# Kernel optimization log

Hardware: AMD Instinct MI355X
Metric: run time of the kernel (lower is better)

The kernel has to match this reference:

```python
import jax, jax.numpy as jnp
import numpy as np

D = 1024
H = 16
DEPTH = D // H


def setup_inputs() -> dict:
    key = jax.random.key(0)
    ks = jax.random.split(key, 9)
    s = 1.0 / np.sqrt(D)
    return {
        "x": jax.random.normal(ks[0], (2, 2048, D), dtype=jnp.float32),
        "Wq": jax.random.uniform(ks[1], (D, D), jnp.float32, -s, s),
        "bq": jax.random.uniform(ks[2], (D,), jnp.float32, -s, s),
        "Wk": jax.random.uniform(ks[3], (D, D), jnp.float32, -s, s),
        "bk": jax.random.uniform(ks[4], (D,), jnp.float32, -s, s),
        "Wv": jax.random.uniform(ks[5], (D, D), jnp.float32, -s, s),
        "bv": jax.random.uniform(ks[6], (D,), jnp.float32, -s, s),
        "Wo": jax.random.uniform(ks[7], (D, D), jnp.float32, -s, s),
        "bo": jax.random.uniform(ks[8], (D,), jnp.float32, -s, s),
    }


def _split_heads(t):
    b, s, _ = t.shape
    return t.reshape(b, s, H, DEPTH).transpose(0, 2, 1, 3)  # [B,H,S,depth]


def reference(x, Wq, bq, Wk, bk, Wv, bv, Wo, bo):
    q = _split_heads(x @ Wq.T + bq)
    k = _split_heads(x @ Wk.T + bk)
    v = _split_heads(x @ Wv.T + bv)
    scores = jnp.einsum("bhqd,bhkd->bhqk", q, k) / jnp.sqrt(jnp.float32(DEPTH))
    weights = jax.nn.softmax(scores, axis=-1)
    attn = jnp.einsum("bhqk,bhkd->bhqd", weights, v)
    b, _, s, _ = attn.shape
    attn = attn.transpose(0, 2, 1, 3).reshape(b, s, D)
    return attn @ Wo.T + bo
```

## Files before the change

### kernel.cpp

```cpp
#include <hip/hip_runtime.h>
#include <hip/hip_bf16.h>


typedef __bf16 bf16x8 __attribute__((ext_vector_type(8)));
typedef float f32x4 __attribute__((ext_vector_type(4)));
typedef unsigned short u16;
typedef unsigned short u16x4 __attribute__((ext_vector_type(4)));
typedef unsigned short u16x8 __attribute__((ext_vector_type(8)));
typedef unsigned int u32x2 __attribute__((ext_vector_type(2)));

__device__ __forceinline__ u16 f2bf(float f) {
  union { float f; unsigned u; } x; x.f = f;
  return (u16)((x.u + 0x7fffu + ((x.u >> 16) & 1u)) >> 16);
}

__device__ __forceinline__ void load_lds16(const void* g, void* l) {
  __builtin_amdgcn_global_load_lds((const __attribute__((address_space(1))) void*)g,
                                   (__attribute__((address_space(3))) void*)l,
                                   16, 0, 0);
}

__device__ __forceinline__ bf16x8 frag128(const u16* base, int row, int ch) {
  return *(const bf16x8*)((const char*)base + row * 128 + (((ch) ^ (row & 7)) << 4));
}

__device__ __forceinline__ float exp2_hw(float x) {
  float r;
  asm("v_exp_f32 %0, %1" : "=v"(r) : "v"(x));
  return r;
}

__device__ __forceinline__ unsigned cvt_pk_bf16(float lo, float hi) {
  unsigned r;
  asm("v_cvt_pk_bf16_f32 %0, %1, %2" : "=v"(r) : "v"(lo), "v"(hi));
  return r;
}

__device__ __forceinline__ bf16x8 mk8(unsigned a, unsigned b, unsigned c,
                                      unsigned d) {
  union { unsigned u[4]; bf16x8 v; } x;
  x.u[0] = a; x.u[1] = b; x.u[2] = c; x.u[3] = d;
  return x.v;
}

__global__ __launch_bounds__(256) void cvt_all(
    const float* __restrict__ x, const float* __restrict__ wq,
    const float* __restrict__ wk, const float* __restrict__ wv,
    const float* __restrict__ wo, u16* __restrict__ dst) {
  int i = blockIdx.x * 256 + threadIdx.x;
  const float* src;
  int loc;
  if (i < 1048576) {
    src = x; loc = i;
  } else {
    int j = i - 1048576;
    int seg = j >> 18;
    loc = j & 262143;
    src = (seg == 0) ? wq : (seg == 1) ? wk : (seg == 2) ? wv : wo;
  }
  f32x4 v = ((const f32x4*)src)[loc];
  u16x4 o;
#pragma unroll
  for (int j = 0; j < 4; ++j) o[j] = f2bf(v[j]);
  ((u16x4*)dst)[i] = o;
}

template <int BM, int MODE>
__global__ __launch_bounds__(256) void gemm_bf16(
    const u16* __restrict__ A, const u16* __restrict__ Bw,
    const float* __restrict__ bias0, const float* __restrict__ bias1,
    const float* __restrict__ bias2,
    u16* __restrict__ o_q, u16* __restrict__ o_k, u16* __restrict__ o_vt,
    float* __restrict__ o_f, int K) {
  constexpr int MBF = BM / 32;
  constexpr int NBX = (MODE == 0) ? 24 : 8;
  constexpr int NBY = (MODE == 0) ? 32 : 64;
  __shared__ u16 sA[BM * 64];
  __shared__ u16 sB[128 * 64];
  const int tid = threadIdx.x, l = tid & 63, w = tid >> 6;
  const int wr = w >> 1, wc = w & 1;
  const int lr = l & 15, lq = l >> 4;
  const int lin = blockIdx.y * NBX + blockIdx.x;
  const int wgs = (lin & 7) * (NBX * NBY / 8) + (lin >> 3);
  const int m0 = (wgs / NBX) * BM, n0 = (wgs % NBX) * 128;

  f32x4 acc[MBF][4];
#pragma unroll
  for (int mb = 0; mb < MBF; ++mb)
#pragma unroll
    for (int nb = 0; nb < 4; ++nb) acc[mb][nb] = f32x4{0.f, 0.f, 0.f, 0.f};

  const int nkt = K / 64;
  for (int kt = 0; kt < nkt; ++kt) {
#pragma unroll
    for (int i = 0; i < BM / 32; ++i) {
      int p = (i * 4 + w) * 1024 + l * 16;
      int row = p >> 7, ch = ((p >> 4) & 7) ^ (row & 7);
      load_lds16(A + (size_t)(m0 + row) * K + kt * 64 + ch * 8,
                 (char*)sA + (i * 4 + w) * 1024);
    }
#pragma unroll
    for (int i = 0; i < 4; ++i) {
      int p = (i * 4 + w) * 1024 + l * 16;
      int row = p >> 7, ch = ((p >> 4) & 7) ^ (row & 7);
      load_lds16(Bw + (size_t)(n0 + row) * K + kt * 64 + ch * 8,
                 (char*)sB + (i * 4 + w) * 1024);
    }
    __syncthreads();
#pragma unroll
    for (int ks = 0; ks < 2; ++ks) {
      bf16x8 af[MBF], bfr[4];
#pragma unroll
      for (int mb = 0; mb < MBF; ++mb)
        af[mb] = frag128(sA, wr * (BM / 2) + mb * 16 + lr, lq + 4 * ks);
#pragma unroll
      for (int nb = 0; nb < 4; ++nb)
        bfr[nb] = frag128(sB, wc * 64 + nb * 16 + lr, lq + 4 * ks);
#pragma unroll
      for (int mb = 0; mb < MBF; ++mb)
#pragma unroll
        for (int nb = 0; nb < 4; ++nb)
          acc[mb][nb] = __builtin_amdgcn_mfma_f32_16x16x32_bf16(
              af[mb], bfr[nb], acc[mb][nb], 0, 0, 0);
    }
    __syncthreads();
  }

#pragma unroll
  for (int nb = 0; nb < 4; ++nb) {
    const int n = n0 + wc * 64 + nb * 16 + lr;
    if constexpr (MODE == 0) {
      const int qkv = n >> 10, c = n & 1023;
      const float* bp = (qkv == 0) ? bias0 : ((qkv == 1) ? bias1 : bias2);
      const float bv = bp[c];
      const int h = c >> 6, d = c & 63;
      if (qkv == 2) {
#pragma unroll
        for (int mb = 0; mb < MBF; ++mb) {
          int mbase = m0 + wr * (BM / 2) + mb * 16 + lq * 4;
          int b = mbase >> 11, s0 = mbase & 2047;
          int pos0 = (s0 & ~31) | (((s0 >> 2) & 3) << 3) | (((s0 >> 4) & 1) << 2);
          u16x4 pk;
#pragma unroll
          for (int r = 0; r < 4; ++r) pk[r] = f2bf(acc[mb][nb][r] + bv);
          *(u16x4*)(o_vt + ((size_t)((b * 16 + h) * 64 + d)) * 2048 + pos0) = pk;
        }
      } else {
        u16* dp = (qkv == 0) ? o_q : o_k;
#pragma unroll
        for (int mb = 0; mb < MBF; ++mb)
#pragma unroll
          for (int r = 0; r < 4; ++r) {
            int m = m0 + wr * (BM / 2) + mb * 16 + lq * 4 + r;
            int b = m >> 11, s = m & 2047;
            float v = acc[mb][nb][r] + bv;
            if (qkv == 0) v *= 0.18033688011f;
            dp[((size_t)(b * 16 + h) * 2048 + s) * 64 + d] = f2bf(v);
          }
      }
    } else {
      const float bv = bias0[n];
#pragma unroll
      for (int mb = 0; mb < MBF; ++mb)
#pragma unroll
        for (int r = 0; r < 4; ++r) {
          int m = m0 + wr * (BM / 2) + mb * 16 + lq * 4 + r;
          o_f[(size_t)m * 1024 + n] = acc[mb][nb][r] + bv;
        }
    }
  }
}

__global__ __launch_bounds__(256, 2) void attn_fwd(
    const u16* __restrict__ q16, const u16* __restrict__ k16,
    const u16* __restrict__ vt16, u16* __restrict__ att16) {
  __shared__ u16 sK[2][128 * 64];
  __shared__ u16 sV[2][64 * 128];
  const int tid = threadIdx.x, l = tid & 63, w = tid >> 6;
  const int lr = l & 15, lq = l >> 4;
  const int lin = (blockIdx.y << 4) | blockIdx.x;
  const int wg = (lin & 7) * 64 + (lin >> 3);
  const int qt = wg & 15, bh = wg >> 4;
  const int b = bh >> 4, h = bh & 15;
  const char* kg = (const char*)(k16 + (size_t)bh * 2048 * 64);
  const char* vg = (const char*)(vt16 + (size_t)bh * 64 * 2048);

  bf16x8 aq[2][2];
#pragma unroll
  for (int mb = 0; mb < 2; ++mb)
#pragma unroll
    for (int ks = 0; ks < 2; ++ks) {
      int qrow = qt * 128 + w * 32 + mb * 16 + lr;
      aq[mb][ks] = *(const bf16x8*)(q16 + ((size_t)bh * 2048 + qrow) * 64 +
                                    ks * 32 + lq * 8);
    }

  int koff[4], voff[4];
#pragma unroll
  for (int i = 0; i < 4; ++i) {
    int p = (i * 4 + w) * 1024 + l * 16;
    int krow = p >> 7, kch = ((p >> 4) & 7) ^ (krow & 7);
    koff[i] = krow * 128 + kch * 16;
    int vrow = p >> 8, vch = ((p >> 4) & 15) ^ (vrow & 7);
    voff[i] = vrow * 4096 + vch * 16;
  }

#pragma unroll
  for (int i = 0; i < 4; ++i)
    load_lds16(kg + koff[i], (char*)sK[0] + (i * 4 + w) * 1024);
#pragma unroll
  for (int i = 0; i < 4; ++i)
    load_lds16(vg + voff[i], (char*)sV[0] + (i * 4 + w) * 1024);
  __syncthreads();

  f32x4 o[2][4];
#pragma unroll
  for (int mb = 0; mb < 2; ++mb)
#pragma unroll
    for (int db = 0; db < 4; ++db) o[mb][db] = f32x4{0.f, 0.f, 0.f, 0.f};
  float l_run[2] = {0.f, 0.f};

  for (int kt = 0; kt < 16; ++kt) {
    const int cur = kt & 1;
    const u16* sKc = sK[cur];
    const u16* sVc = sV[cur];

    if (kt < 15) {
      char* dK = (char*)sK[cur ^ 1];
      char* dV = (char*)sV[cur ^ 1];
#pragma unroll
      for (int i = 0; i < 4; ++i)
        load_lds16(kg + (size_t)(kt + 1) * 16384 + koff[i],
                   dK + (i * 4 + w) * 1024);
#pragma unroll
      for (int i = 0; i < 4; ++i)
        load_lds16(vg + (size_t)(kt + 1) * 256 + voff[i],
                   dV + (i * 4 + w) * 1024);
    }

    f32x4 s[2][8];
#pragma unroll
    for (int mb = 0; mb < 2; ++mb)
#pragma unroll
      for (int nb = 0; nb < 8; ++nb) s[mb][nb] = f32x4{0.f, 0.f, 0.f, 0.f};
    __builtin_amdgcn_s_setprio(1);
#pragma unroll
    for (int ks = 0; ks < 2; ++ks) {
#pragma unroll
      for (int g = 0; g < 2; ++g) {
        bf16x8 bk[4];
#pragma unroll
        for (int j = 0; j < 4; ++j)
          bk[j] = frag128(sKc, (g * 4 + j) * 16 + lr, lq + 4 * ks);
#pragma unroll
        for (int j = 0; j < 4; ++j)
#pragma unroll
          for (int mb = 0; mb < 2; ++mb)
            s[mb][g * 4 + j] = __builtin_amdgcn_mfma_f32_16x16x32_bf16(
                bk[j], aq[mb][ks], s[mb][g * 4 + j], 0, 0, 0);
      }
    }
    __builtin_amdgcn_s_setprio(0);

#pragma unroll
    for (int mb = 0; mb < 2; ++mb) {
      float rs = 0.f;
#pragma unroll
      for (int nb = 0; nb < 8; ++nb)
#pragma unroll
        for (int r = 0; r < 4; ++r) {
          float p_ = exp2_hw(s[mb][nb][r]);
          s[mb][nb][r] = p_;
          rs += p_;
        }
      l_run[mb] += rs;
    }

#pragma unroll
    for (int g = 0; g < 4; ++g) {
      bf16x8 ap[2];
#pragma unroll
      for (int mb = 0; mb < 2; ++mb)
        ap[mb] = mk8(cvt_pk_bf16(s[mb][2 * g][0], s[mb][2 * g][1]),
                     cvt_pk_bf16(s[mb][2 * g][2], s[mb][2 * g][3]),
                     cvt_pk_bf16(s[mb][2 * g + 1][0], s[mb][2 * g + 1][1]),
                     cvt_pk_bf16(s[mb][2 * g + 1][2], s[mb][2 * g + 1][3]));
      bf16x8 bv[4];
#pragma unroll
      for (int db = 0; db < 4; ++db) {
        int row = db * 16 + lr;
        bv[db] = *(const bf16x8*)((const char*)sVc + row * 256 +
                                  (((4 * g + lq) ^ (row & 7)) << 4));
      }
      __builtin_amdgcn_s_setprio(1);
#pragma unroll
      for (int db = 0; db < 4; ++db)
#pragma unroll
        for (int mb = 0; mb < 2; ++mb)
          o[mb][db] = __builtin_amdgcn_mfma_f32_16x16x32_bf16(
              ap[mb], bv[db], o[mb][db], 0, 0, 0);
      __builtin_amdgcn_s_setprio(0);
    }

    __syncthreads();
  }

#pragma unroll
  for (int mb = 0; mb < 2; ++mb) {
    float lv = l_run[mb];
    lv += __shfl_xor(lv, 16, 64);
    lv += __shfl_xor(lv, 32, 64);
    float inv[4];
#pragma unroll
    for (int r = 0; r < 4; ++r) inv[r] = 1.f / __shfl(lv, lq * 4 + r, 64);
#pragma unroll
    for (int db = 0; db < 4; ++db)
#pragma unroll
      for (int r = 0; r < 4; ++r) {
        float v = o[mb][db][r] * inv[r];
        int qg_ = qt * 128 + w * 32 + mb * 16 + lq * 4 + r;
        int col = h * 64 + db * 16 + lr;
        att16[((size_t)(b * 2048 + qg_)) * 1024 + col] = f2bf(v);
      }
  }
}

extern "C" void kernel_launch(void* const* d_in, const int* in_sizes, int n_in,
                              void* d_out, int out_size, void* d_ws, size_t ws_size,
                              hipStream_t stream) {
  const float* x  = (const float*)d_in[0];
  const float* Wq = (const float*)d_in[1];
  const float* bq = (const float*)d_in[2];
  const float* Wk = (const float*)d_in[3];
  const float* bk = (const float*)d_in[4];
  const float* Wv = (const float*)d_in[5];
  const float* bv = (const float*)d_in[6];
  const float* Wo = (const float*)d_in[7];
  const float* bo = (const float*)d_in[8];
  float* out = (float*)d_out;

  char* ws = (char*)d_ws;
  const size_t MB = 1024 * 1024;
  if (ws_size < 40 * MB) return;
  u16* x16  = (u16*)(ws);
  u16* w16  = (u16*)(ws + 8 * MB);
  u16* q16  = (u16*)(ws + 16 * MB);
  u16* k16  = (u16*)(ws + 24 * MB);
  u16* vt16 = (u16*)(ws + 32 * MB);
  u16* att16 = x16;

  cvt_all<<<8192, 256, 0, stream>>>(x, Wq, Wk, Wv, Wo, x16);

  gemm_bf16<128, 0><<<dim3(24, 32), 256, 0, stream>>>(
      x16, w16, bq, bk, bv, q16, k16, vt16, nullptr, 1024);

  attn_fwd<<<dim3(16, 32), 256, 0, stream>>>(q16, k16, vt16, att16);

  gemm_bf16<64, 1><<<dim3(8, 64), 256, 0, stream>>>(
      att16, w16 + 3145728, bo, nullptr, nullptr, nullptr, nullptr, nullptr,
      out, 1024);
}
```

Measured before the change: 107.5 us.

## Software-pipeline attention loop: overlap PV of previous tile with QK of current

```diff
diff --git a/kernel.cpp b/kernel.cpp
--- a/kernel.cpp
+++ b/kernel.cpp
@@ -175,7 +175,7 @@
     const u16* __restrict__ q16, const u16* __restrict__ k16,
     const u16* __restrict__ vt16, u16* __restrict__ att16) {
   __shared__ u16 sK[2][128 * 64];
-  __shared__ u16 sV[2][64 * 128];
+  __shared__ u16 sV[3][64 * 128];
   const int tid = threadIdx.x, l = tid & 63, w = tid >> 6;
   const int lr = l & 15, lq = l >> 4;
   const int lin = (blockIdx.y << 4) | blockIdx.x;
@@ -219,24 +219,23 @@
 #pragma unroll
     for (int db = 0; db < 4; ++db) o[mb][db] = f32x4{0.f, 0.f, 0.f, 0.f};
   float l_run[2] = {0.f, 0.f};
-
-  for (int kt = 0; kt < 16; ++kt) {
-    const int cur = kt & 1;
-    const u16* sKc = sK[cur];
-    const u16* sVc = sV[cur];
-
-    if (kt < 15) {
-      char* dK = (char*)sK[cur ^ 1];
-      char* dV = (char*)sV[cur ^ 1];
+  bf16x8 pE[2][4], pO[2][4];
+
+#pragma unroll
+  for (int t = 0; t < 16; ++t) {
+    if (t < 15) {
+      char* dK = (char*)sK[(t + 1) & 1];
+      char* dV = (char*)sV[(t + 1) % 3];
 #pragma unroll
       for (int i = 0; i < 4; ++i)
-        load_lds16(kg + (size_t)(kt + 1) * 16384 + koff[i],
+        load_lds16(kg + (size_t)(t + 1) * 16384 + koff[i],
                    dK + (i * 4 + w) * 1024);
 #pragma unroll
       for (int i = 0; i < 4; ++i)
-        load_lds16(vg + (size_t)(kt + 1) * 256 + voff[i],
+        load_lds16(vg + (size_t)(t + 1) * 256 + voff[i],
                    dV + (i * 4 + w) * 1024);
     }
+    const u16* sKc = sK[t & 1];
 
     f32x4 s[2][8];
 #pragma unroll
@@ -261,6 +260,29 @@
       }
     }
     __builtin_amdgcn_s_setprio(0);
+
+    if (t > 0) {
+      const u16* sVp = sV[(t - 1) % 3];
+#pragma unroll
+      for (int g = 0; g < 4; ++g) {
+        bf16x8 bv[4];
+#pragma unroll
+        for (int db = 0; db < 4; ++db) {
+          int row = db * 16 + lr;
+          bv[db] = *(const bf16x8*)((const char*)sVp + row * 256 +
+                                    (((4 * g + lq) ^ (row & 7)) << 4));
+        }
+        __builtin_amdgcn_s_setprio(1);
+#pragma unroll
+        for (int db = 0; db < 4; ++db)
+#pragma unroll
+          for (int mb = 0; mb < 2; ++mb)
+            o[mb][db] = __builtin_amdgcn_mfma_f32_16x16x32_bf16(
+                ((t - 1) & 1) ? pO[mb][g] : pE[mb][g], bv[db], o[mb][db],
+                0, 0, 0);
+        __builtin_amdgcn_s_setprio(0);
+      }
+    }
 
 #pragma unroll
     for (int mb = 0; mb < 2; ++mb) {
@@ -274,35 +296,37 @@
           rs += p_;
         }
       l_run[mb] += rs;
-    }
-
+#pragma unroll
+      for (int g = 0; g < 4; ++g) {
+        bf16x8 pk = mk8(cvt_pk_bf16(s[mb][2 * g][0], s[mb][2 * g][1]),
+                        cvt_pk_bf16(s[mb][2 * g][2], s[mb][2 * g][3]),
+                        cvt_pk_bf16(s[mb][2 * g + 1][0], s[mb][2 * g + 1][1]),
+                        cvt_pk_bf16(s[mb][2 * g + 1][2], s[mb][2 * g + 1][3]));
+        if (t & 1) pO[mb][g] = pk; else pE[mb][g] = pk;
+      }
+    }
+
+    __syncthreads();
+  }
+
+  {
+    const u16* sVp = sV[0];
 #pragma unroll
     for (int g = 0; g < 4; ++g) {
-      bf16x8 ap[2];
-#pragma unroll
-      for (int mb = 0; mb < 2; ++mb)
-        ap[mb] = mk8(cvt_pk_bf16(s[mb][2 * g][0], s[mb][2 * g][1]),
-                     cvt_pk_bf16(s[mb][2 * g][2], s[mb][2 * g][3]),
-                     cvt_pk_bf16(s[mb][2 * g + 1][0], s[mb][2 * g + 1][1]),
-                     cvt_pk_bf16(s[mb][2 * g + 1][2], s[mb][2 * g + 1][3]));
       bf16x8 bv[4];
 #pragma unroll
       for (int db = 0; db < 4; ++db) {
         int row = db * 16 + lr;
-        bv[db] = *(const bf16x8*)((const char*)sVc + row * 256 +
+        bv[db] = *(const bf16x8*)((const char*)sVp + row * 256 +
                                   (((4 * g + lq) ^ (row & 7)) << 4));
       }
-      __builtin_amdgcn_s_setprio(1);
 #pragma unroll
       for (int db = 0; db < 4; ++db)
 #pragma unroll
         for (int mb = 0; mb < 2; ++mb)
           o[mb][db] = __builtin_amdgcn_mfma_f32_16x16x32_bf16(
-              ap[mb], bv[db], o[mb][db], 0, 0, 0);
-      __builtin_amdgcn_s_setprio(0);
-    }
-
-    __syncthreads();
+              pO[mb][g], bv[db], o[mb][db], 0, 0, 0);
+    }
   }
 
 #pragma unroll
```

New measurement: 415.4 us. 3.87x slower.

## Split key tile into halves and interleave QK^T of second half with PV of first

Applied to the files above, without the earlier changes.

```diff
diff --git a/kernel.cpp b/kernel.cpp
--- a/kernel.cpp
+++ b/kernel.cpp
@@ -238,69 +238,121 @@
                    dV + (i * 4 + w) * 1024);
     }
 
-    f32x4 s[2][8];
+    f32x4 sA[2][4];
 #pragma unroll
     for (int mb = 0; mb < 2; ++mb)
 #pragma unroll
-      for (int nb = 0; nb < 8; ++nb) s[mb][nb] = f32x4{0.f, 0.f, 0.f, 0.f};
+      for (int nb = 0; nb < 4; ++nb) sA[mb][nb] = f32x4{0.f, 0.f, 0.f, 0.f};
     __builtin_amdgcn_s_setprio(1);
 #pragma unroll
     for (int ks = 0; ks < 2; ++ks) {
-#pragma unroll
-      for (int g = 0; g < 2; ++g) {
-        bf16x8 bk[4];
-#pragma unroll
-        for (int j = 0; j < 4; ++j)
-          bk[j] = frag128(sKc, (g * 4 + j) * 16 + lr, lq + 4 * ks);
-#pragma unroll
-        for (int j = 0; j < 4; ++j)
-#pragma unroll
-          for (int mb = 0; mb < 2; ++mb)
-            s[mb][g * 4 + j] = __builtin_amdgcn_mfma_f32_16x16x32_bf16(
-                bk[j], aq[mb][ks], s[mb][g * 4 + j], 0, 0, 0);
-      }
+      bf16x8 bk[4];
+#pragma unroll
+      for (int j = 0; j < 4; ++j)
+        bk[j] = frag128(sKc, j * 16 + lr, lq + 4 * ks);
+#pragma unroll
+      for (int j = 0; j < 4; ++j)
+#pragma unroll
+        for (int mb = 0; mb < 2; ++mb)
+          sA[mb][j] = __builtin_amdgcn_mfma_f32_16x16x32_bf16(
+              bk[j], aq[mb][ks], sA[mb][j], 0, 0, 0);
     }
     __builtin_amdgcn_s_setprio(0);
 
+    bf16x8 pA[2][2];
 #pragma unroll
     for (int mb = 0; mb < 2; ++mb) {
       float rs = 0.f;
 #pragma unroll
-      for (int nb = 0; nb < 8; ++nb)
+      for (int nb = 0; nb < 4; ++nb)
 #pragma unroll
         for (int r = 0; r < 4; ++r) {
-          float p_ = exp2_hw(s[mb][nb][r]);
-          s[mb][nb][r] = p_;
+          float p_ = exp2_hw(sA[mb][nb][r]);
+          sA[mb][nb][r] = p_;
           rs += p_;
         }
       l_run[mb] += rs;
-    }
-
-#pragma unroll
-    for (int g = 0; g < 4; ++g) {
-      bf16x8 ap[2];
-#pragma unroll
-      for (int mb = 0; mb < 2; ++mb)
-        ap[mb] = mk8(cvt_pk_bf16(s[mb][2 * g][0], s[mb][2 * g][1]),
-                     cvt_pk_bf16(s[mb][2 * g][2], s[mb][2 * g][3]),
-                     cvt_pk_bf16(s[mb][2 * g + 1][0], s[mb][2 * g + 1][1]),
-                     cvt_pk_bf16(s[mb][2 * g + 1][2], s[mb][2 * g + 1][3]));
+#pragma unroll
+      for (int g = 0; g < 2; ++g)
+        pA[mb][g] = mk8(cvt_pk_bf16(sA[mb][2 * g][0], sA[mb][2 * g][1]),
+                        cvt_pk_bf16(sA[mb][2 * g][2], sA[mb][2 * g][3]),
+                        cvt_pk_bf16(sA[mb][2 * g + 1][0], sA[mb][2 * g + 1][1]),
+                        cvt_pk_bf16(sA[mb][2 * g + 1][2], sA[mb][2 * g + 1][3]));
+    }
+
+    f32x4 sB[2][4];
+#pragma unroll
+    for (int mb = 0; mb < 2; ++mb)
+#pragma unroll
+      for (int nb = 0; nb < 4; ++nb) sB[mb][nb] = f32x4{0.f, 0.f, 0.f, 0.f};
+    __builtin_amdgcn_s_setprio(1);
+#pragma unroll
+    for (int ks = 0; ks < 2; ++ks) {
+      bf16x8 bk[4];
+#pragma unroll
+      for (int j = 0; j < 4; ++j)
+        bk[j] = frag128(sKc, (4 + j) * 16 + lr, lq + 4 * ks);
+      bf16x8 bvA[4];
+#pragma unroll
+      for (int db = 0; db < 4; ++db) {
+        int row = db * 16 + lr;
+        bvA[db] = *(const bf16x8*)((const char*)sVc + row * 256 +
+                                   (((4 * ks + lq) ^ (row & 7)) << 4));
+      }
+#pragma unroll
+      for (int j = 0; j < 4; ++j)
+#pragma unroll
+        for (int mb = 0; mb < 2; ++mb)
+          sB[mb][j] = __builtin_amdgcn_mfma_f32_16x16x32_bf16(
+              bk[j], aq[mb][ks], sB[mb][j], 0, 0, 0);
+#pragma unroll
+      for (int db = 0; db < 4; ++db)
+#pragma unroll
+        for (int mb = 0; mb < 2; ++mb)
+          o[mb][db] = __builtin_amdgcn_mfma_f32_16x16x32_bf16(
+              pA[mb][ks], bvA[db], o[mb][db], 0, 0, 0);
+    }
+    __builtin_amdgcn_s_setprio(0);
+
+    bf16x8 pB[2][2];
+#pragma unroll
+    for (int mb = 0; mb < 2; ++mb) {
+      float rs = 0.f;
+#pragma unroll
+      for (int nb = 0; nb < 4; ++nb)
+#pragma unroll
+        for (int r = 0; r < 4; ++r) {
+          float p_ = exp2_hw(sB[mb][nb][r]);
+          sB[mb][nb][r] = p_;
+          rs += p_;
+        }
+      l_run[mb] += rs;
+#pragma unroll
+      for (int g = 0; g < 2; ++g)
+        pB[mb][g] = mk8(cvt_pk_bf16(sB[mb][2 * g][0], sB[mb][2 * g][1]),
+                        cvt_pk_bf16(sB[mb][2 * g][2], sB[mb][2 * g][3]),
+                        cvt_pk_bf16(sB[mb][2 * g + 1][0], sB[mb][2 * g + 1][1]),
+                        cvt_pk_bf16(sB[mb][2 * g + 1][2], sB[mb][2 * g + 1][3]));
+    }
+
+    __builtin_amdgcn_s_setprio(1);
+#pragma unroll
+    for (int g2 = 0; g2 < 2; ++g2) {
       bf16x8 bv[4];
 #pragma unroll
       for (int db = 0; db < 4; ++db) {
         int row = db * 16 + lr;
         bv[db] = *(const bf16x8*)((const char*)sVc + row * 256 +
-                                  (((4 * g + lq) ^ (row & 7)) << 4));
+                                  (((4 * (2 + g2) + lq) ^ (row & 7)) << 4));
       }
-      __builtin_amdgcn_s_setprio(1);
 #pragma unroll
       for (int db = 0; db < 4; ++db)
 #pragma unroll
         for (int mb = 0; mb < 2; ++mb)
           o[mb][db] = __builtin_amdgcn_mfma_f32_16x16x32_bf16(
-              ap[mb], bv[db], o[mb][db], 0, 0, 0);
-      __builtin_amdgcn_s_setprio(0);
-    }
+              pB[mb][g2], bv[db], o[mb][db], 0, 0, 0);
+    }
+    __builtin_amdgcn_s_setprio(0);
 
     __syncthreads();
   }
```

Measured after the change: 108.2 us. No clear change (+0.7%).
